# Kernel tuning notes

Measured on AMD Instinct MI355X. Metric: run time of the kernel, lower is better.

## Reference

```python
import jax, jax.numpy as jnp
import numpy as np

BS, Q, NC, M = 16, 900, 91, 1600
EPS = 1e-8

def setup_inputs() -> dict:
    key = jax.random.key(0)
    k1, k2, k3, k4 = jax.random.split(key, 4)
    return {
        "pred_logits": jax.random.normal(k1, (BS, Q, NC), dtype=jnp.float32),
        "pred_boxes": jax.random.uniform(k2, (BS, Q, 4), dtype=jnp.float32),
        "tgt_ids": jax.random.randint(k3, (M,), 0, NC, dtype=jnp.int64),
        "tgt_bbox": jax.random.uniform(k4, (M, 4), dtype=jnp.float32),
    }

def _cxcywh_to_xyxy(b):
    cx, cy, w, h = b[..., 0], b[..., 1], b[..., 2], b[..., 3]
    return jnp.stack([cx - 0.5 * w, cy - 0.5 * h, cx + 0.5 * w, cy + 0.5 * h], axis=-1)

def _generalized_box_iou(boxes1, boxes2):
    # boxes: xyxy. Pairwise GIoU: [N, M]
    area1 = (boxes1[:, 2] - boxes1[:, 0]) * (boxes1[:, 3] - boxes1[:, 1])
    area2 = (boxes2[:, 2] - boxes2[:, 0]) * (boxes2[:, 3] - boxes2[:, 1])
    lt = jnp.maximum(boxes1[:, None, :2], boxes2[None, :, :2])
    rb = jnp.minimum(boxes1[:, None, 2:], boxes2[None, :, 2:])
    wh = jnp.clip(rb - lt, 0.0)
    inter = wh[..., 0] * wh[..., 1]
    union = area1[:, None] + area2[None, :] - inter
    iou = inter / union
    lt_e = jnp.minimum(boxes1[:, None, :2], boxes2[None, :, :2])
    rb_e = jnp.maximum(boxes1[:, None, 2:], boxes2[None, :, 2:])
    wh_e = jnp.clip(rb_e - lt_e, 0.0)
    area_e = wh_e[..., 0] * wh_e[..., 1]
    return iou - (area_e - union) / area_e

def reference(pred_logits, pred_boxes, tgt_ids, tgt_bbox):
    cost_class_w, cost_bbox_w, cost_giou_w = 1.0, 1.0, 1.0
    alpha, gamma = 0.25, 2.0
    bs, nq, nc = pred_logits.shape
    out_prob = jax.nn.sigmoid(pred_logits.reshape(bs * nq, nc))  # [N, C]
    out_bbox = pred_boxes.reshape(bs * nq, 4)  # [N, 4]
    # focal classification cost
    neg_cost = (1.0 - alpha) * out_prob ** gamma * (-jnp.log1p(-out_prob + EPS))
    pos_cost = alpha * (1.0 - out_prob) ** gamma * (-jnp.log(out_prob + EPS))
    cost_class = (pos_cost - neg_cost)[:, tgt_ids]  # [N, M]
    # L1 cdist
    cost_bbox = jnp.sum(jnp.abs(out_bbox[:, None, :] - tgt_bbox[None, :, :]), axis=-1)
    # GIoU cost
    cost_giou = -_generalized_box_iou(_cxcywh_to_xyxy(out_bbox), _cxcywh_to_xyxy(tgt_bbox))
    C = cost_bbox_w * cost_bbox + cost_class_w * cost_class + cost_giou_w * cost_giou
    return C.reshape(bs, nq, -1)
```

## Files before the change

kernel.cpp:

```cpp
#include <hip/hip_runtime.h>
#include <cstddef>

#define NROWS 14400
#define NCLS  91
#define MTGT  1600
#define RPB   8
#define TPB   320

__global__ __launch_bounds__(TPB) void matcher_cost_kernel(
    const float* __restrict__ logits,
    const float* __restrict__ boxes,
    const int*   __restrict__ tids,
    const float* __restrict__ tbox,
    float*       __restrict__ out)
{
    __shared__ float s_cc[RPB * NCLS];
    const int row0 = blockIdx.x * RPB;
    const int t = threadIdx.x;

    for (int i = t; i < RPB * NCLS; i += TPB) {
        const int r = i / NCLS;
        const int c = i - r * NCLS;
        const float x = logits[(size_t)(row0 + r) * NCLS + c];
        const float p = 1.0f / (1.0f + __expf(-x));
        const float omp = 1.0f - p;
        const float neg = 0.75f * p * p * (-log1pf(-p + 1e-8f));
        const float pos = 0.25f * omp * omp * (-logf(p + 1e-8f));
        s_cc[i] = pos - neg;
    }
    __syncthreads();

    float4 pb[RPB];
    const float4* bx4 = reinterpret_cast<const float4*>(boxes);
#pragma unroll
    for (int r = 0; r < RPB; ++r) pb[r] = bx4[row0 + r];

    const float4* tb4 = reinterpret_cast<const float4*>(tbox);
    for (int m = t; m < MTGT; m += TPB) {
        const float4 tb = tb4[m];
        const int id = tids[m];
        const float tx0 = tb.x - 0.5f * tb.z, tx1 = tb.x + 0.5f * tb.z;
        const float ty0 = tb.y - 0.5f * tb.w, ty1 = tb.y + 0.5f * tb.w;
        const float ta  = tb.z * tb.w;
#pragma unroll
        for (int r = 0; r < RPB; ++r) {
            const float cc = s_cc[r * NCLS + id];
            const float4 p = pb[r];
            const float l1 = fabsf(p.x - tb.x) + fabsf(p.y - tb.y)
                           + fabsf(p.z - tb.z) + fabsf(p.w - tb.w);
            const float px0 = p.x - 0.5f * p.z, px1 = p.x + 0.5f * p.z;
            const float py0 = p.y - 0.5f * p.w, py1 = p.y + 0.5f * p.w;
            const float pa  = p.z * p.w;
            const float iw = fminf(px1, tx1) - fmaxf(px0, tx0);
            const float ih = fminf(py1, ty1) - fmaxf(py0, ty0);
            const float inter = fmaxf(iw, 0.0f) * fmaxf(ih, 0.0f);
            const float uni = pa + ta - inter;
            const float iou = inter * __builtin_amdgcn_rcpf(uni);
            const float ew = fmaxf(px1, tx1) - fminf(px0, tx0);
            const float eh = fmaxf(py1, ty1) - fminf(py0, ty0);
            const float ea = ew * eh;
            const float giou = iou - (ea - uni) * __builtin_amdgcn_rcpf(ea);
            out[(size_t)(row0 + r) * MTGT + m] = l1 + cc - giou;
        }
    }
}

extern "C" void kernel_launch(void* const* d_in, const int* in_sizes, int n_in,
                              void* d_out, int out_size, void* d_ws, size_t ws_size,
                              hipStream_t stream) {
    const float* logits = (const float*)d_in[0];
    const float* boxes  = (const float*)d_in[1];
    const int*   tids   = (const int*)d_in[2];
    const float* tbox   = (const float*)d_in[3];
    float* out = (float*)d_out;

    dim3 grid(NROWS / RPB);
    dim3 block(TPB);
    hipLaunchKernelGGL(matcher_cost_kernel, grid, block, 0, stream,
                       logits, boxes, tids, tbox, out);
}
```

Measured before the change: 134.3 us.

## Split class-cost prep into separate kernel and vectorize pair-cost stores

```diff
diff --git a/kernel.cpp b/kernel.cpp
--- a/kernel.cpp
+++ b/kernel.cpp
@@ -4,65 +4,100 @@
 #define NROWS 14400
 #define NCLS  91
 #define MTGT  1600
-#define RPB   8
-#define TPB   320
+#define NG    400
+#define RPT   2
+#define TPB   256
+#define TBL   (NROWS * NCLS)
+#define NTHREADS ((NROWS / RPT) * NG)
+#define PREP_BLOCKS ((TBL + TPB - 1) / TPB)
+#define PAIR_BLOCKS (NTHREADS / TPB)
 
-__global__ __launch_bounds__(TPB) void matcher_cost_kernel(
-    const float* __restrict__ logits,
+__global__ __launch_bounds__(TPB) void prep_kernel(
+    const float* __restrict__ logits, float* __restrict__ cc)
+{
+    const int gid = blockIdx.x * TPB + threadIdx.x;
+    if (gid >= TBL) return;
+    const float x = logits[gid];
+    const float p = 1.0f / (1.0f + __expf(-x));
+    const float omp = 1.0f - p;
+    const float neg = 0.75f * p * p * (-log1pf(-p + 1e-8f));
+    const float pos = 0.25f * omp * omp * (-logf(p + 1e-8f));
+    cc[gid] = pos - neg + 1.0f;
+}
+
+__global__ __launch_bounds__(TPB) void pair_kernel(
     const float* __restrict__ boxes,
     const int*   __restrict__ tids,
     const float* __restrict__ tbox,
+    const float* __restrict__ cc,
     float*       __restrict__ out)
 {
-    __shared__ float s_cc[RPB * NCLS];
-    const int row0 = blockIdx.x * RPB;
-    const int t = threadIdx.x;
+    const int gid = blockIdx.x * TPB + threadIdx.x;
+    const int rp  = gid / NG;
+    const int g   = gid - rp * NG;
+    const int row0 = rp * RPT;
 
-    for (int i = t; i < RPB * NCLS; i += TPB) {
-        const int r = i / NCLS;
-        const int c = i - r * NCLS;
-        const float x = logits[(size_t)(row0 + r) * NCLS + c];
-        const float p = 1.0f / (1.0f + __expf(-x));
-        const float omp = 1.0f - p;
-        const float neg = 0.75f * p * p * (-log1pf(-p + 1e-8f));
-        const float pos = 0.25f * omp * omp * (-logf(p + 1e-8f));
-        s_cc[i] = pos - neg;
-    }
-    __syncthreads();
+    const float4* bx4 = reinterpret_cast<const float4*>(boxes);
+    const float4 pA = bx4[row0];
+    const float4 pB = bx4[row0 + 1];
+    const float pAx0 = pA.x - 0.5f * pA.z, pAx1 = pA.x + 0.5f * pA.z;
+    const float pAy0 = pA.y - 0.5f * pA.w, pAy1 = pA.y + 0.5f * pA.w;
+    const float pAa  = pA.z * pA.w;
+    const float pBx0 = pB.x - 0.5f * pB.z, pBx1 = pB.x + 0.5f * pB.z;
+    const float pBy0 = pB.y - 0.5f * pB.w, pBy1 = pB.y + 0.5f * pB.w;
+    const float pBa  = pB.z * pB.w;
 
-    float4 pb[RPB];
-    const float4* bx4 = reinterpret_cast<const float4*>(boxes);
-#pragma unroll
-    for (int r = 0; r < RPB; ++r) pb[r] = bx4[row0 + r];
+    const int4 idv = reinterpret_cast<const int4*>(tids)[g];
+    const int ida[4] = { idv.x, idv.y, idv.z, idv.w };
+    const float* ccA = cc + (size_t)row0 * NCLS;
+    const float* ccB = ccA + NCLS;
 
     const float4* tb4 = reinterpret_cast<const float4*>(tbox);
-    for (int m = t; m < MTGT; m += TPB) {
-        const float4 tb = tb4[m];
-        const int id = tids[m];
+    float rA[4], rB[4];
+#pragma unroll
+    for (int j = 0; j < 4; ++j) {
+        const float4 tb = tb4[g * 4 + j];
         const float tx0 = tb.x - 0.5f * tb.z, tx1 = tb.x + 0.5f * tb.z;
         const float ty0 = tb.y - 0.5f * tb.w, ty1 = tb.y + 0.5f * tb.w;
         const float ta  = tb.z * tb.w;
-#pragma unroll
-        for (int r = 0; r < RPB; ++r) {
-            const float cc = s_cc[r * NCLS + id];
-            const float4 p = pb[r];
-            const float l1 = fabsf(p.x - tb.x) + fabsf(p.y - tb.y)
-                           + fabsf(p.z - tb.z) + fabsf(p.w - tb.w);
-            const float px0 = p.x - 0.5f * p.z, px1 = p.x + 0.5f * p.z;
-            const float py0 = p.y - 0.5f * p.w, py1 = p.y + 0.5f * p.w;
-            const float pa  = p.z * p.w;
-            const float iw = fminf(px1, tx1) - fmaxf(px0, tx0);
-            const float ih = fminf(py1, ty1) - fmaxf(py0, ty0);
+        const float ccj_a = ccA[ida[j]];
+        const float ccj_b = ccB[ida[j]];
+
+        {
+            const float l1 = fabsf(pA.x - tb.x) + fabsf(pA.y - tb.y)
+                           + fabsf(pA.z - tb.z) + fabsf(pA.w - tb.w);
+            const float iw = fminf(pAx1, tx1) - fmaxf(pAx0, tx0);
+            const float ih = fminf(pAy1, ty1) - fmaxf(pAy0, ty0);
             const float inter = fmaxf(iw, 0.0f) * fmaxf(ih, 0.0f);
-            const float uni = pa + ta - inter;
-            const float iou = inter * __builtin_amdgcn_rcpf(uni);
-            const float ew = fmaxf(px1, tx1) - fminf(px0, tx0);
-            const float eh = fmaxf(py1, ty1) - fminf(py0, ty0);
+            const float uni = pAa + ta - inter;
+            const float ew = fmaxf(pAx1, tx1) - fminf(pAx0, tx0);
+            const float eh = fmaxf(pAy1, ty1) - fminf(pAy0, ty0);
             const float ea = ew * eh;
-            const float giou = iou - (ea - uni) * __builtin_amdgcn_rcpf(ea);
-            out[(size_t)(row0 + r) * MTGT + m] = l1 + cc - giou;
+            const float num  = fmaf(inter, ea, uni * uni);
+            const float rden = __builtin_amdgcn_rcpf(uni * ea);
+            rA[j] = l1 + ccj_a - num * rden;
+        }
+        {
+            const float l1 = fabsf(pB.x - tb.x) + fabsf(pB.y - tb.y)
+                           + fabsf(pB.z - tb.z) + fabsf(pB.w - tb.w);
+            const float iw = fminf(pBx1, tx1) - fmaxf(pBx0, tx0);
+            const float ih = fminf(pBy1, ty1) - fmaxf(pBy0, ty0);
+            const float inter = fmaxf(iw, 0.0f) * fmaxf(ih, 0.0f);
+            const float uni = pBa + ta - inter;
+            const float ew = fmaxf(pBx1, tx1) - fminf(pBx0, tx0);
+            const float eh = fmaxf(pBy1, ty1) - fminf(pBy0, ty0);
+            const float ea = ew * eh;
+            const float num  = fmaf(inter, ea, uni * uni);
+            const float rden = __builtin_amdgcn_rcpf(uni * ea);
+            rB[j] = l1 + ccj_b - num * rden;
         }
     }
+
+    float4* out4 = reinterpret_cast<float4*>(out);
+    const float4 oA = { rA[0], rA[1], rA[2], rA[3] };
+    const float4 oB = { rB[0], rB[1], rB[2], rB[3] };
+    out4[(size_t)row0 * NG + g]       = oA;
+    out4[(size_t)(row0 + 1) * NG + g] = oB;
 }
 
 extern "C" void kernel_launch(void* const* d_in, const int* in_sizes, int n_in,
@@ -72,10 +107,11 @@
     const float* boxes  = (const float*)d_in[1];
     const int*   tids   = (const int*)d_in[2];
     const float* tbox   = (const float*)d_in[3];
-    float* out = (float*)d_out;
+    float* outp = (float*)d_out;
+    float* cc   = (float*)d_ws;
 
-    dim3 grid(NROWS / RPB);
-    dim3 block(TPB);
-    hipLaunchKernelGGL(matcher_cost_kernel, grid, block, 0, stream,
-                       logits, boxes, tids, tbox, out);
+    hipLaunchKernelGGL(prep_kernel, dim3(PREP_BLOCKS), dim3(TPB), 0, stream,
+                       logits, cc);
+    hipLaunchKernelGGL(pair_kernel, dim3(PAIR_BLOCKS), dim3(TPB), 0, stream,
+                       boxes, tids, tbox, cc, outp);
 }
```

After: 130.5 us. -2.8%, faster.
